# Kernel optimization log

Hardware: AMD Instinct MI355X
Metric: run time of the kernel (lower is better)

## Reference

```python
import jax, jax.numpy as jnp
import numpy as np

B, N, D, KD = 8, 2048, 64, 64

def setup_inputs() -> dict:
    key = jax.random.key(0)
    ks = jax.random.split(key, 7)
    s = 1.0 / np.sqrt(D)
    return {
        "x":  jax.random.normal(ks[0], (B, N, D), dtype=jnp.float32),
        "Wq": jax.random.normal(ks[1], (D, KD), dtype=jnp.float32) * s,
        "bq": jnp.zeros((KD,), jnp.float32),
        "Wk": jax.random.normal(ks[2], (D, KD), dtype=jnp.float32) * s,
        "bk": jnp.zeros((KD,), jnp.float32),
        "Wv": jax.random.normal(ks[3], (D, KD), dtype=jnp.float32) * s,
        "bv": jnp.zeros((KD,), jnp.float32),
    }

def reference(x, Wq, bq, Wk, bk, Wv, bv):
    # Q,K,V: [B,N,KD]
    Q = x @ Wq + bq
    K = x @ Wk + bk
    V = x @ Wv + bv
    # scores: [B,N,N] (note: original applies NO 1/sqrt(d) scaling)
    scores = jnp.einsum('bij,bkj->bik', Q, K)
    probs = jax.nn.softmax(scores, axis=-1)
    # mean-threshold sparsification: keep entries above the row mean
    mask = (probs > jnp.mean(probs, axis=-1, keepdims=True)).astype(probs.dtype)
    sparse = probs * mask
    out = jnp.einsum('bij,bjk->bik', sparse, V)  # [B,N,KD]
    return out
```

## Files before the change

### kernel.cpp

```cpp
#include <hip/hip_runtime.h>

#define NB 8
#define NS 2048
#define ND 64
#define LOG2E 1.44269504f

typedef _Float16 half8 __attribute__((ext_vector_type(8)));
typedef __attribute__((ext_vector_type(4))) float floatx4;

__device__ __forceinline__ half8 cvt8(const float* p) {
    float4 a = *(const float4*)p;
    float4 b = *(const float4*)(p + 4);
    half8 h = {(_Float16)a.x, (_Float16)a.y, (_Float16)a.z, (_Float16)a.w,
               (_Float16)b.x, (_Float16)b.y, (_Float16)b.z, (_Float16)b.w};
    return h;
}
__device__ __forceinline__ half8 cvtWcol(const float* base) {
    half8 h;
#pragma unroll
    for (int j = 0; j < 8; ++j) h[j] = (_Float16)base[j * 64];
    return h;
}

__global__ __launch_bounds__(256) void qkv_proj(
    const float* __restrict__ x,
    const float* __restrict__ Wq, const float* __restrict__ bq,
    const float* __restrict__ Wk, const float* __restrict__ bk,
    const float* __restrict__ Wv, const float* __restrict__ bv,
    _Float16* __restrict__ Qg, _Float16* __restrict__ Kg,
    _Float16* __restrict__ Vt)
{
    __shared__ _Float16 vt[64 * 18];

    const int tid  = threadIdx.x;
    const int wv   = tid >> 6;
    const int l    = tid & 63;
    const int quad = l >> 4;
    const int tx   = l & 15;

    const int b  = blockIdx.x & 7;
    const int n0 = (blockIdx.x >> 3) * 16;

    const float* xr = x + ((size_t)b * NS + n0 + tx) * ND + quad * 8;
    half8 a0 = cvt8(xr);
    half8 a1 = cvt8(xr + 32);

    const floatx4 zf = {0.f, 0.f, 0.f, 0.f};

#pragma unroll
    for (int i = 0; i < 3; ++i) {
        const int ct = wv * 3 + i;
        const int m  = ct >> 2;
        const int lcol = (ct & 3) * 16 + tx;

        const float* Wm;
        const float* Bm;
        if (m == 0)      { Wm = Wq; Bm = bq; }
        else if (m == 1) { Wm = Wk; Bm = bk; }
        else             { Wm = Wv; Bm = bv; }

        half8 b0 = cvtWcol(Wm + (quad * 8) * 64 + lcol);
        half8 b1 = cvtWcol(Wm + (32 + quad * 8) * 64 + lcol);

        floatx4 acc = __builtin_amdgcn_mfma_f32_16x16x32_f16(a0, b0, zf, 0, 0, 0);
        acc = __builtin_amdgcn_mfma_f32_16x16x32_f16(a1, b1, acc, 0, 0, 0);
        const float bias = Bm[lcol];

        if (m == 0) {
#pragma unroll
            for (int r = 0; r < 4; ++r)
                Qg[((size_t)b * NS + n0 + quad * 4 + r) * ND + lcol] =
                    (_Float16)((acc[r] + bias) * LOG2E);
        } else if (m == 1) {
#pragma unroll
            for (int r = 0; r < 4; ++r)
                Kg[((size_t)b * NS + n0 + quad * 4 + r) * ND + lcol] = (_Float16)(acc[r] + bias);
        } else {
#pragma unroll
            for (int r = 0; r < 4; ++r)
                vt[lcol * 18 + quad * 4 + r] = (_Float16)(acc[r] + bias);
        }
    }
    __syncthreads();
    {
        const int d = tid >> 2, seg = tid & 3;
        uint2 p = *(uint2*)&vt[d * 18 + seg * 4];
        *(uint2*)(Vt + ((size_t)b * ND + d) * NS + n0 + seg * 4) = p;
    }
}

__global__ __launch_bounds__(512, 2) void attn(
    const _Float16* __restrict__ Qg,
    const _Float16* __restrict__ Kg,
    const _Float16* __restrict__ Vt,
    float* __restrict__ out)
{
    __shared__ _Float16 ksm[2 * 64 * 76];
    __shared__ _Float16 vsm[2 * 64 * 76];
    __shared__ _Float16 psm[32 * 76];
    __shared__ float lsh[128];

    const int tid  = threadIdx.x;
    const int wv   = tid >> 6;
    const int l    = tid & 63;
    const int quad = l >> 4;
    const int tx   = l & 15;
    const int h    = wv >> 2;
    const int kq   = wv & 3;

    const int b  = blockIdx.x & 7;
    const int q0 = (blockIdx.x >> 3) * 32;

    const _Float16* Qb = Qg + ((size_t)b * NS + q0 + h * 16) * ND;
    const _Float16* Kb = Kg + (size_t)b * NS * ND;
    const _Float16* Vb = Vt + (size_t)b * ND * NS;

    half8 qf0 = *(const half8*)(Qb + (size_t)tx * ND + quad * 8);
    half8 qf1 = *(const half8*)(Qb + (size_t)tx * ND + 32 + quad * 8);

    const int skey = tid >> 3;
    const int sc   = (tid & 7) * 8;
    const _Float16* Ksrc = Kb + (size_t)skey * ND + sc;
    const _Float16* Vsrc = Vb + (size_t)skey * NS + sc;
    const int sdst = skey * 76 + sc;

    const floatx4 zf = {0.f, 0.f, 0.f, 0.f};
    const int krow = (kq * 16 + tx) * 76;

    float lacc[4] = {0.f, 0.f, 0.f, 0.f};
    {
        uint4 gk = *(const uint4*)Ksrc;
        *(uint4*)(ksm + sdst) = gk;
        for (int t = 0; t < 32; ++t) {
            const int buf = (t & 1) * 4864;
            __syncthreads();
            if (t < 31) gk = *(const uint4*)(Ksrc + (size_t)(t + 1) * 64 * ND);
            half8 kf0 = *(const half8*)(ksm + buf + krow + quad * 8);
            half8 kf1 = *(const half8*)(ksm + buf + krow + 32 + quad * 8);
            floatx4 c = __builtin_amdgcn_mfma_f32_16x16x32_f16(qf0, kf0, zf, 0, 0, 0);
            c = __builtin_amdgcn_mfma_f32_16x16x32_f16(qf1, kf1, c, 0, 0, 0);
#pragma unroll
            for (int r = 0; r < 4; ++r)
                lacc[r] += __builtin_amdgcn_exp2f(c[r]);
            if (t < 31) *(uint4*)(ksm + (buf ^ 4864) + sdst) = gk;
        }
    }
#pragma unroll
    for (int off = 1; off < 16; off <<= 1)
#pragma unroll
        for (int r = 0; r < 4; ++r)
            lacc[r] += __shfl_xor(lacc[r], off);
    if (tx == 0) {
#pragma unroll
        for (int r = 0; r < 4; ++r)
            lsh[kq * 32 + h * 16 + quad * 4 + r] = lacc[r];
    }

    uint4 gk2 = *(const uint4*)Ksrc;
    uint4 gv  = *(const uint4*)Vsrc;
    __syncthreads();

    float inv[4], thr[4];
#pragma unroll
    for (int r = 0; r < 4; ++r) {
        const int row = h * 16 + quad * 4 + r;
        float L = lsh[row] + lsh[32 + row] + lsh[64 + row] + lsh[96 + row];
        inv[r] = 1.f / L;
        thr[r] = L * (1.f / (float)NS);
    }

    *(uint4*)(ksm + sdst) = gk2;
    *(uint4*)(vsm + sdst) = gv;
    floatx4 o = zf;

    for (int t = 0; t < 32; ++t) {
        const int buf = (t & 1) * 4864;
        __syncthreads();
        if (t < 31) {
            gk2 = *(const uint4*)(Ksrc + (size_t)(t + 1) * 64 * ND);
            gv  = *(const uint4*)(Vsrc + (size_t)(t + 1) * 64);
        }
        half8 kf0 = *(const half8*)(ksm + buf + krow + quad * 8);
        half8 kf1 = *(const half8*)(ksm + buf + krow + 32 + quad * 8);
        floatx4 c = __builtin_amdgcn_mfma_f32_16x16x32_f16(qf0, kf0, zf, 0, 0, 0);
        c = __builtin_amdgcn_mfma_f32_16x16x32_f16(qf1, kf1, c, 0, 0, 0);
#pragma unroll
        for (int r = 0; r < 4; ++r) {
            float e = __builtin_amdgcn_exp2f(c[r]);
            float w = (e > thr[r]) ? e * inv[r] : 0.f;
            psm[(h * 16 + quad * 4 + r) * 76 + kq * 16 + tx] = (_Float16)w;
        }
        __syncthreads();
#pragma unroll
        for (int ck = 0; ck < 2; ++ck) {
            half8 vf = *(const half8*)(vsm + buf + krow + ck * 32 + quad * 8);
            half8 af = *(const half8*)(psm + (h * 16 + tx) * 76 + ck * 32 + quad * 8);
            o = __builtin_amdgcn_mfma_f32_16x16x32_f16(af, vf, o, 0, 0, 0);
        }
        if (t < 31) {
            *(uint4*)(ksm + (buf ^ 4864) + sdst) = gk2;
            *(uint4*)(vsm + (buf ^ 4864) + sdst) = gv;
        }
    }

#pragma unroll
    for (int r = 0; r < 4; ++r)
        out[((size_t)b * NS + q0 + h * 16 + quad * 4 + r) * ND + kq * 16 + tx] = o[r];
}

extern "C" void kernel_launch(void* const* d_in, const int* in_sizes, int n_in,
                              void* d_out, int out_size, void* d_ws, size_t ws_size,
                              hipStream_t stream) {
    const float* x  = (const float*)d_in[0];
    const float* Wq = (const float*)d_in[1];
    const float* bq = (const float*)d_in[2];
    const float* Wk = (const float*)d_in[3];
    const float* bk = (const float*)d_in[4];
    const float* Wv = (const float*)d_in[5];
    const float* bv = (const float*)d_in[6];

    _Float16* Qg = (_Float16*)d_ws;
    _Float16* Kg = Qg + (size_t)NB * NS * ND;
    _Float16* Vt = Kg + (size_t)NB * NS * ND;

    qkv_proj<<<NB * (NS / 16), 256, 0, stream>>>(x, Wq, bq, Wk, bk, Wv, bv, Qg, Kg, Vt);
    attn<<<NB * (NS / 32), 512, 0, stream>>>(Qg, Kg, Vt, (float*)d_out);
}
```

Baseline: 109.9 us.

## Keep probabilities in registers and split PV over key quarters with LDS reduction

The QK^T MFMA now has K and Q operands swapped, so each lane holds four key scores for a single query row. The thresholded probabilities can then be passed straight into a 16x16x16 MFMA against V as the B operand, which removes the psm shared buffer and the second __syncthreads inside each tile. Each wave accumulates a partial output over its own quarter of the keys for all 64 output dims. The four partials are summed at the end through an LDS buffer that aliases the K/V buffers, with vectorized float4 stores. This trades a barrier and LDS round-trip per tile for four accumulators per wave, narrower MFMAs and a final cross-wave reduction.

```diff
diff --git a/kernel.cpp b/kernel.cpp
--- a/kernel.cpp
+++ b/kernel.cpp
@@ -4,8 +4,11 @@
 #define NS 2048
 #define ND 64
 #define LOG2E 1.44269504f
+#define SP 76
+#define KBUF (64 * SP)
 
 typedef _Float16 half8 __attribute__((ext_vector_type(8)));
+typedef _Float16 half4 __attribute__((ext_vector_type(4)));
 typedef __attribute__((ext_vector_type(4))) float floatx4;
 
 __device__ __forceinline__ half8 cvt8(const float* p) {
@@ -95,10 +98,11 @@
     const _Float16* __restrict__ Vt,
     float* __restrict__ out)
 {
-    __shared__ _Float16 ksm[2 * 64 * 76];
-    __shared__ _Float16 vsm[2 * 64 * 76];
-    __shared__ _Float16 psm[32 * 76];
+    __shared__ __align__(16) _Float16 smraw[4 * KBUF];
     __shared__ float lsh[128];
+    _Float16* ksm = smraw;
+    _Float16* vsm = smraw + 2 * KBUF;
+    float*    obuf = (float*)smraw;
 
     const int tid  = threadIdx.x;
     const int wv   = tid >> 6;
@@ -122,90 +126,92 @@
     const int sc   = (tid & 7) * 8;
     const _Float16* Ksrc = Kb + (size_t)skey * ND + sc;
     const _Float16* Vsrc = Vb + (size_t)skey * NS + sc;
-    const int sdst = skey * 76 + sc;
+    const int sdst = skey * SP + sc;
 
     const floatx4 zf = {0.f, 0.f, 0.f, 0.f};
-    const int krow = (kq * 16 + tx) * 76;
-
-    float lacc[4] = {0.f, 0.f, 0.f, 0.f};
+    const int krow = (kq * 16 + tx) * SP;
+
+    float lacc = 0.f;
     {
         uint4 gk = *(const uint4*)Ksrc;
         *(uint4*)(ksm + sdst) = gk;
         for (int t = 0; t < 32; ++t) {
-            const int buf = (t & 1) * 4864;
+            const _Float16* kb_ = ksm + (t & 1) * KBUF;
             __syncthreads();
             if (t < 31) gk = *(const uint4*)(Ksrc + (size_t)(t + 1) * 64 * ND);
-            half8 kf0 = *(const half8*)(ksm + buf + krow + quad * 8);
-            half8 kf1 = *(const half8*)(ksm + buf + krow + 32 + quad * 8);
-            floatx4 c = __builtin_amdgcn_mfma_f32_16x16x32_f16(qf0, kf0, zf, 0, 0, 0);
-            c = __builtin_amdgcn_mfma_f32_16x16x32_f16(qf1, kf1, c, 0, 0, 0);
-#pragma unroll
-            for (int r = 0; r < 4; ++r)
-                lacc[r] += __builtin_amdgcn_exp2f(c[r]);
-            if (t < 31) *(uint4*)(ksm + (buf ^ 4864) + sdst) = gk;
-        }
-    }
-#pragma unroll
-    for (int off = 1; off < 16; off <<= 1)
-#pragma unroll
-        for (int r = 0; r < 4; ++r)
-            lacc[r] += __shfl_xor(lacc[r], off);
-    if (tx == 0) {
-#pragma unroll
-        for (int r = 0; r < 4; ++r)
-            lsh[kq * 32 + h * 16 + quad * 4 + r] = lacc[r];
-    }
+            half8 kf0 = *(const half8*)(kb_ + krow + quad * 8);
+            half8 kf1 = *(const half8*)(kb_ + krow + 32 + quad * 8);
+            floatx4 c = __builtin_amdgcn_mfma_f32_16x16x32_f16(kf0, qf0, zf, 0, 0, 0);
+            c = __builtin_amdgcn_mfma_f32_16x16x32_f16(kf1, qf1, c, 0, 0, 0);
+            lacc += __builtin_amdgcn_exp2f(c[0]) + __builtin_amdgcn_exp2f(c[1])
+                  + __builtin_amdgcn_exp2f(c[2]) + __builtin_amdgcn_exp2f(c[3]);
+            if (t < 31) *(uint4*)(ksm + ((t & 1) ^ 1) * KBUF + sdst) = gk;
+        }
+    }
+    lacc += __shfl_xor(lacc, 16);
+    lacc += __shfl_xor(lacc, 32);
+    if (l < 16) lsh[wv * 16 + l] = lacc;
 
     uint4 gk2 = *(const uint4*)Ksrc;
     uint4 gv  = *(const uint4*)Vsrc;
     __syncthreads();
 
-    float inv[4], thr[4];
-#pragma unroll
-    for (int r = 0; r < 4; ++r) {
-        const int row = h * 16 + quad * 4 + r;
-        float L = lsh[row] + lsh[32 + row] + lsh[64 + row] + lsh[96 + row];
-        inv[r] = 1.f / L;
-        thr[r] = L * (1.f / (float)NS);
-    }
+    float L = lsh[(h * 4 + 0) * 16 + tx] + lsh[(h * 4 + 1) * 16 + tx]
+            + lsh[(h * 4 + 2) * 16 + tx] + lsh[(h * 4 + 3) * 16 + tx];
+    const float inv = 1.f / L;
+    const float thr = L * (1.f / (float)NS);
 
     *(uint4*)(ksm + sdst) = gk2;
     *(uint4*)(vsm + sdst) = gv;
-    floatx4 o = zf;
+    floatx4 o[4] = {zf, zf, zf, zf};
 
     for (int t = 0; t < 32; ++t) {
-        const int buf = (t & 1) * 4864;
+        const _Float16* kb_ = ksm + (t & 1) * KBUF;
+        const _Float16* vb_ = vsm + (t & 1) * KBUF;
         __syncthreads();
         if (t < 31) {
             gk2 = *(const uint4*)(Ksrc + (size_t)(t + 1) * 64 * ND);
             gv  = *(const uint4*)(Vsrc + (size_t)(t + 1) * 64);
         }
-        half8 kf0 = *(const half8*)(ksm + buf + krow + quad * 8);
-        half8 kf1 = *(const half8*)(ksm + buf + krow + 32 + quad * 8);
-        floatx4 c = __builtin_amdgcn_mfma_f32_16x16x32_f16(qf0, kf0, zf, 0, 0, 0);
-        c = __builtin_amdgcn_mfma_f32_16x16x32_f16(qf1, kf1, c, 0, 0, 0);
+        half8 kf0 = *(const half8*)(kb_ + krow + quad * 8);
+        half8 kf1 = *(const half8*)(kb_ + krow + 32 + quad * 8);
+        floatx4 c = __builtin_amdgcn_mfma_f32_16x16x32_f16(kf0, qf0, zf, 0, 0, 0);
+        c = __builtin_amdgcn_mfma_f32_16x16x32_f16(kf1, qf1, c, 0, 0, 0);
+        half4 w;
 #pragma unroll
         for (int r = 0; r < 4; ++r) {
             float e = __builtin_amdgcn_exp2f(c[r]);
-            float w = (e > thr[r]) ? e * inv[r] : 0.f;
-            psm[(h * 16 + quad * 4 + r) * 76 + kq * 16 + tx] = (_Float16)w;
-        }
-        __syncthreads();
-#pragma unroll
-        for (int ck = 0; ck < 2; ++ck) {
-            half8 vf = *(const half8*)(vsm + buf + krow + ck * 32 + quad * 8);
-            half8 af = *(const half8*)(psm + (h * 16 + tx) * 76 + ck * 32 + quad * 8);
-            o = __builtin_amdgcn_mfma_f32_16x16x32_f16(af, vf, o, 0, 0, 0);
+            w[r] = (e > thr) ? (_Float16)(e * inv) : (_Float16)0.f;
+        }
+#pragma unroll
+        for (int dt = 0; dt < 4; ++dt) {
+            half4 vf = *(const half4*)(vb_ + (dt * 16 + tx) * SP + kq * 16 + quad * 4);
+            o[dt] = __builtin_amdgcn_mfma_f32_16x16x16f16(vf, w, o[dt], 0, 0, 0);
         }
         if (t < 31) {
-            *(uint4*)(ksm + (buf ^ 4864) + sdst) = gk2;
-            *(uint4*)(vsm + (buf ^ 4864) + sdst) = gv;
-        }
-    }
-
-#pragma unroll
-    for (int r = 0; r < 4; ++r)
-        out[((size_t)b * NS + q0 + h * 16 + quad * 4 + r) * ND + kq * 16 + tx] = o[r];
+            *(uint4*)(ksm + ((t & 1) ^ 1) * KBUF + sdst) = gk2;
+            *(uint4*)(vsm + ((t & 1) ^ 1) * KBUF + sdst) = gv;
+        }
+    }
+
+    __syncthreads();
+#pragma unroll
+    for (int dt = 0; dt < 4; ++dt)
+        *(floatx4*)(obuf + wv * (16 * 68) + tx * 68 + dt * 16 + quad * 4) = o[dt];
+    __syncthreads();
+
+    {
+        const int row = tid >> 4;
+        const int c4  = (tid & 15) * 4;
+        const int hh  = row >> 4, rl = row & 15;
+        float4 s = {0.f, 0.f, 0.f, 0.f};
+#pragma unroll
+        for (int k2 = 0; k2 < 4; ++k2) {
+            float4 v = *(float4*)(obuf + ((hh * 4 + k2) * 16 + rl) * 68 + c4);
+            s.x += v.x; s.y += v.y; s.z += v.z; s.w += v.w;
+        }
+        *(float4*)(out + ((size_t)b * NS + q0 + row) * ND + c4) = s;
+    }
 }
 
 extern "C" void kernel_launch(void* const* d_in, const int* in_sizes, int n_in,
```

New measurement: 161.3 us. 1.47x slower.
